# Kernel optimization log

Hardware: AMD Instinct MI355X
Metric: run time of the kernel (lower is better)

Reference implementation:

```python
import jax, jax.numpy as jnp
import numpy as np

B, S, H = 4, 2048, 1024
NH, HD = 16, 64
WIN = 64  # window_size = min(64, seq_len)
SCALE = float(np.sqrt(HD))


def setup_inputs() -> dict:
    key = jax.random.key(0)
    ks = jax.random.split(key, 10)
    w = lambda k, shp: (jax.random.normal(k, shp, jnp.float32) * 0.02)
    return {
        "x": jax.random.normal(ks[0], (B, S, H), jnp.float32),
        "attention_mask": jnp.ones((B, S), jnp.int32),
        "Wq": w(ks[1], (H, NH * HD)), "bq": jnp.zeros((NH * HD,), jnp.float32),
        "Wk": w(ks[2], (H, NH * HD)), "bk": jnp.zeros((NH * HD,), jnp.float32),
        "Wv": w(ks[3], (H, NH * HD)), "bv": jnp.zeros((NH * HD,), jnp.float32),
        "Wo": w(ks[4], (NH * HD, H)), "bo": jnp.zeros((H,), jnp.float32),
    }


def reference(x, attention_mask, Wq, bq, Wk, bk, Wv, bv, Wo, bo):
    # projections -> [B, NH, S, HD]
    def split_heads(t):
        return t.reshape(B, S, NH, HD).transpose(0, 2, 1, 3)
    q = split_heads(x @ Wq + bq)
    k = split_heads(x @ Wk + bk)
    v = split_heads(x @ Wv + bv)

    scores = jnp.einsum("bhqd,bhkd->bhqk", q, k) / SCALE  # [B,NH,S,S]

    # local banded mask: |i - j| <= window_size // 2
    idx = jnp.arange(S)
    local = jnp.abs(idx[None, :] - idx[:, None]) <= (WIN // 2)  # [S,S]
    scores = jnp.where(local[None, None, :, :], scores, -jnp.inf)

    # padding mask: [B,1,1,S]
    scores = jnp.where(attention_mask[:, None, None, :] == 0, -jnp.inf, scores)

    probs = jax.nn.softmax(scores, axis=-1)
    probs = jnp.nan_to_num(probs)  # rows that are fully masked -> 0

    out = jnp.einsum("bhqk,bhkd->bhqd", probs, v)
    out = out.transpose(0, 2, 1, 3).reshape(B, S, NH * HD)
    return out @ Wo + bo
```

## Files before the change

### kernel.cpp

```cpp
#include <hip/hip_runtime.h>
#include <stdint.h>

typedef unsigned short u16;
typedef __attribute__((ext_vector_type(8))) short short8;
typedef __attribute__((ext_vector_type(4))) float f32x4;

#define S_LEN 2048
#define HID   1024
#define QKV_LD 3072
#define M_ROWS 8192

__device__ __forceinline__ u16 f2bf(float f) {
  unsigned u = __float_as_uint(f);
  unsigned r = (u + 0x7fffu + ((u >> 16) & 1u)) >> 16;
  return (u16)r;
}

__device__ __forceinline__ void gload16(const u16* g, u16* l) {
  __builtin_amdgcn_global_load_lds(
      (const __attribute__((address_space(1))) unsigned int*)(g),
      (__attribute__((address_space(3))) unsigned int*)(l),
      16, 0, 0);
}

__global__ __launch_bounds__(256) void cvt_f32_to_bf16(
    const float* __restrict__ in, u16* __restrict__ out, int n) {
  int i = (blockIdx.x * 256 + threadIdx.x) * 8;
  if (i + 8 > n) return;
  float4 a = *(const float4*)(in + i);
  float4 b = *(const float4*)(in + i + 4);
  u16 t[8];
  t[0] = f2bf(a.x); t[1] = f2bf(a.y); t[2] = f2bf(a.z); t[3] = f2bf(a.w);
  t[4] = f2bf(b.x); t[5] = f2bf(b.y); t[6] = f2bf(b.z); t[7] = f2bf(b.w);
  *(short8*)(out + i) = *(short8*)t;
}

__global__ __launch_bounds__(256) void transpose_to_bf16(
    const float* __restrict__ in, u16* __restrict__ out, int K, int N) {
  __shared__ float tile[32][33];
  int tx = threadIdx.x & 31, ty = threadIdx.x >> 5;
  int n0 = blockIdx.x * 32, k0 = blockIdx.y * 32;
#pragma unroll
  for (int i = 0; i < 32; i += 8)
    tile[ty + i][tx] = in[(size_t)(k0 + ty + i) * N + n0 + tx];
  __syncthreads();
#pragma unroll
  for (int i = 0; i < 32; i += 8)
    out[(size_t)(n0 + ty + i) * K + k0 + tx] = f2bf(tile[tx][ty + i]);
}

__global__ __launch_bounds__(256) void pack_bias(
    const float* __restrict__ bq, const float* __restrict__ bk,
    const float* __restrict__ bv, float* __restrict__ out) {
  int i = blockIdx.x * 256 + threadIdx.x;
  if (i >= 3072) return;
  out[i] = (i < 1024) ? bq[i] : (i < 2048) ? bk[i - 1024] : bv[i - 2048];
}

template<int OUT_BF16>
__global__ __launch_bounds__(256, 2) void gemm_bt(
    const u16* __restrict__ A, const u16* __restrict__ Bt,
    const float* __restrict__ bias, void* __restrict__ Cout,
    int M, int N, int K) {
  __shared__ __align__(16) u16 Al[128 * 64];
  __shared__ __align__(16) u16 Bl[128 * 64];
  const int tid = threadIdx.x;
  const int wave = tid >> 6, lane = tid & 63;
  const int nbn = N >> 7;
  int wg = blockIdx.x;
  const int cpx = (int)gridDim.x >> 3;
  wg = (wg & 7) * cpx + (wg >> 3);
  const int bm = wg / nbn, bn = wg % nbn;

  const int wm = wave >> 1, wn = wave & 1;
  const int lrow = lane >> 3;
  const int lslot = lane & 7;
  const int gslot = lslot ^ lrow;
  const int qlane = lane & 15, kgrp = lane >> 4;

  size_t a_off[4], b_off[4];
  u16 *al_base[4], *bl_base[4];
#pragma unroll
  for (int t = 0; t < 4; ++t) {
    int rr = (wave * 4 + t) * 8 + lrow;
    a_off[t] = (size_t)(bm * 128 + rr) * K + gslot * 8;
    b_off[t] = (size_t)(bn * 128 + rr) * K + gslot * 8;
    al_base[t] = Al + (wave * 4 + t) * 512;
    bl_base[t] = Bl + (wave * 4 + t) * 512;
  }

  f32x4 acc[4][4] = {};
  for (int kt = 0; kt < K; kt += 64) {
#pragma unroll
    for (int t = 0; t < 4; ++t) {
      gload16(A + a_off[t] + kt, al_base[t]);
      gload16(Bt + b_off[t] + kt, bl_base[t]);
    }
    __syncthreads();
#pragma unroll
    for (int kk = 0; kk < 2; ++kk) {
      short8 af[4], bf[4];
#pragma unroll
      for (int mf = 0; mf < 4; ++mf) {
        int row = wm * 64 + mf * 16 + qlane;
        int s = (kk * 4 + kgrp) ^ (row & 7);
        af[mf] = *(const short8*)&Al[row * 64 + s * 8];
      }
#pragma unroll
      for (int nf = 0; nf < 4; ++nf) {
        int row = wn * 64 + nf * 16 + qlane;
        int s = (kk * 4 + kgrp) ^ (row & 7);
        bf[nf] = *(const short8*)&Bl[row * 64 + s * 8];
      }
#pragma unroll
      for (int mf = 0; mf < 4; ++mf)
#pragma unroll
        for (int nf = 0; nf < 4; ++nf)
          acc[mf][nf] = __builtin_amdgcn_mfma_f32_16x16x32_bf16(
              af[mf], bf[nf], acc[mf][nf], 0, 0, 0);
    }
    __syncthreads();
  }

#pragma unroll
  for (int nf = 0; nf < 4; ++nf) {
    int col = bn * 128 + wn * 64 + nf * 16 + qlane;
    float bv = bias[col];
#pragma unroll
    for (int mf = 0; mf < 4; ++mf) {
      int row0 = bm * 128 + wm * 64 + mf * 16 + kgrp * 4;
#pragma unroll
      for (int r = 0; r < 4; ++r) {
        float v = acc[mf][nf][r] + bv;
        if (OUT_BF16)
          ((u16*)Cout)[(size_t)(row0 + r) * N + col] = f2bf(v);
        else
          ((float*)Cout)[(size_t)(row0 + r) * N + col] = v;
      }
    }
  }
}

__global__ __launch_bounds__(256, 2) void attn_local(
    const u16* __restrict__ qkv, const int* __restrict__ amask,
    u16* __restrict__ aout) {
  __shared__ __align__(16) u16 Kl[192][72];
  __shared__ __align__(16) u16 Vt[64][200];
  __shared__ __align__(16) u16 Pl[4][32][104];

  const int tid = threadIdx.x, wave = tid >> 6, lane = tid & 63;
  const int qlane = lane & 15, kgrp = lane >> 4;
  const int bz = blockIdx.x;
  const int qt = bz & 15, h = (bz >> 4) & 15, b = bz >> 8;
  const int qs0 = qt * 128;
  const int jt = qs0 - 32;
  const size_t rbase = (size_t)b * S_LEN;

  {
    const int r0 = tid >> 3, c0 = (tid & 7) * 8;
#pragma unroll
    for (int p = 0; p < 6; ++p) {
      int row = p * 32 + r0;
      int j = jt + row;
      u16 kv[8], vv[8];
      if (j >= 0 && j < S_LEN) {
        const u16* kp = qkv + (rbase + j) * QKV_LD + HID + h * 64 + c0;
        *(short8*)kv = *(const short8*)kp;
        *(short8*)vv = *(const short8*)(kp + HID);
      } else {
#pragma unroll
        for (int q = 0; q < 8; ++q) { kv[q] = 0; vv[q] = 0; }
      }
      *(short8*)&Kl[row][c0] = *(short8*)kv;
#pragma unroll
      for (int q = 0; q < 8; ++q) Vt[c0 + q][row] = vv[q];
    }
  }

  short8 qf[2][2];
#pragma unroll
  for (int mf = 0; mf < 2; ++mf)
#pragma unroll
    for (int kk = 0; kk < 2; ++kk)
      qf[mf][kk] = *(const short8*)(qkv +
          (rbase + qs0 + wave * 32 + mf * 16 + qlane) * QKV_LD +
          h * 64 + kk * 32 + kgrp * 8);

  __syncthreads();

  f32x4 sc[2][6] = {};
#pragma unroll
  for (int kk = 0; kk < 2; ++kk) {
    short8 kf[6];
#pragma unroll
    for (int nf = 0; nf < 6; ++nf)
      kf[nf] = *(const short8*)&Kl[wave * 32 + nf * 16 + qlane][kk * 32 + kgrp * 8];
#pragma unroll
    for (int mf = 0; mf < 2; ++mf)
#pragma unroll
      for (int nf = 0; nf < 6; ++nf)
        sc[mf][nf] = __builtin_amdgcn_mfma_f32_16x16x32_bf16(
            qf[mf][kk], kf[nf], sc[mf][nf], 0, 0, 0);
  }

  int jcol[6], mv[6];
#pragma unroll
  for (int nf = 0; nf < 6; ++nf) {
    int j = jt + wave * 32 + nf * 16 + qlane;
    jcol[nf] = j;
    mv[nf] = (j >= 0 && j < S_LEN) ? amask[rbase + j] : 0;
  }

  float inv[2][4];
#pragma unroll
  for (int mf = 0; mf < 2; ++mf) {
    const int irow0 = qs0 + wave * 32 + mf * 16 + kgrp * 4;
    float mx[4] = {-1e30f, -1e30f, -1e30f, -1e30f};
#pragma unroll
    for (int r = 0; r < 4; ++r) {
      int i = irow0 + r;
#pragma unroll
      for (int nf = 0; nf < 6; ++nf) {
        int d = i - jcol[nf];
        if (mv[nf] && d >= -32 && d <= 32) mx[r] = fmaxf(mx[r], sc[mf][nf][r]);
      }
    }
#pragma unroll
    for (int m = 1; m < 16; m <<= 1)
#pragma unroll
      for (int r = 0; r < 4; ++r)
        mx[r] = fmaxf(mx[r], __shfl_xor(mx[r], m));
    float sm[4] = {0.f, 0.f, 0.f, 0.f};
#pragma unroll
    for (int r = 0; r < 4; ++r) {
      int i = irow0 + r;
#pragma unroll
      for (int nf = 0; nf < 6; ++nf) {
        int d = i - jcol[nf];
        bool val = mv[nf] && d >= -32 && d <= 32;
        float p = val ? __expf((sc[mf][nf][r] - mx[r]) * 0.125f) : 0.f;
        sc[mf][nf][r] = p;
        sm[r] += p;
      }
    }
#pragma unroll
    for (int m = 1; m < 16; m <<= 1)
#pragma unroll
      for (int r = 0; r < 4; ++r)
        sm[r] += __shfl_xor(sm[r], m);
#pragma unroll
    for (int r = 0; r < 4; ++r)
      inv[mf][r] = sm[r] > 0.f ? 1.f / sm[r] : 0.f;
#pragma unroll
    for (int nf = 0; nf < 6; ++nf)
#pragma unroll
      for (int r = 0; r < 4; ++r)
        Pl[wave][mf * 16 + kgrp * 4 + r][nf * 16 + qlane] = f2bf(sc[mf][nf][r]);
  }
  __syncthreads();

  f32x4 oc[2][4] = {};
#pragma unroll
  for (int ks = 0; ks < 3; ++ks) {
    short8 pa[2], vb[4];
#pragma unroll
    for (int mf = 0; mf < 2; ++mf)
      pa[mf] = *(const short8*)&Pl[wave][mf * 16 + qlane][ks * 32 + kgrp * 8];
#pragma unroll
    for (int nf = 0; nf < 4; ++nf)
      vb[nf] = *(const short8*)&Vt[nf * 16 + qlane][wave * 32 + ks * 32 + kgrp * 8];
#pragma unroll
    for (int mf = 0; mf < 2; ++mf)
#pragma unroll
      for (int nf = 0; nf < 4; ++nf)
        oc[mf][nf] = __builtin_amdgcn_mfma_f32_16x16x32_bf16(
            pa[mf], vb[nf], oc[mf][nf], 0, 0, 0);
  }

#pragma unroll
  for (int mf = 0; mf < 2; ++mf)
#pragma unroll
    for (int nf = 0; nf < 4; ++nf)
#pragma unroll
      for (int r = 0; r < 4; ++r) {
        size_t row = rbase + qs0 + wave * 32 + mf * 16 + kgrp * 4 + r;
        aout[row * HID + h * 64 + nf * 16 + qlane] =
            f2bf(oc[mf][nf][r] * inv[mf][r]);
      }
}

extern "C" void kernel_launch(void* const* d_in, const int* in_sizes, int n_in,
                              void* d_out, int out_size, void* d_ws, size_t ws_size,
                              hipStream_t stream) {
  const float* x  = (const float*)d_in[0];
  const int* amask = (const int*)d_in[1];
  const float* Wq = (const float*)d_in[2];
  const float* bq = (const float*)d_in[3];
  const float* Wk = (const float*)d_in[4];
  const float* bk = (const float*)d_in[5];
  const float* Wv = (const float*)d_in[6];
  const float* bv = (const float*)d_in[7];
  const float* Wo = (const float*)d_in[8];
  const float* bo = (const float*)d_in[9];
  float* out = (float*)d_out;

  char* w = (char*)d_ws;
  u16* xb    = (u16*)w;   w += (size_t)M_ROWS * HID * 2;
  u16* wqkvt = (u16*)w;   w += (size_t)3072 * 1024 * 2;
  u16* wot   = (u16*)w;   w += (size_t)1024 * 1024 * 2;
  float* bqkv = (float*)w; w += 3072 * 4 + 256;
  u16* qkv   = (u16*)w;   w += (size_t)M_ROWS * 3072 * 2;
  u16* aout  = (u16*)w;   w += (size_t)M_ROWS * HID * 2;

  cvt_f32_to_bf16<<<4096, 256, 0, stream>>>(x, xb, M_ROWS * HID);
  dim3 tg(32, 32);
  transpose_to_bf16<<<tg, 256, 0, stream>>>(Wq, wqkvt,                1024, 1024);
  transpose_to_bf16<<<tg, 256, 0, stream>>>(Wk, wqkvt + 1024 * 1024,  1024, 1024);
  transpose_to_bf16<<<tg, 256, 0, stream>>>(Wv, wqkvt + 2048 * 1024,  1024, 1024);
  transpose_to_bf16<<<tg, 256, 0, stream>>>(Wo, wot,                  1024, 1024);
  pack_bias<<<12, 256, 0, stream>>>(bq, bk, bv, bqkv);

  gemm_bt<1><<<64 * 24, 256, 0, stream>>>(xb, wqkvt, bqkv, qkv, M_ROWS, 3072, 1024);
  attn_local<<<1024, 256, 0, stream>>>(qkv, amask, aout);
  gemm_bt<0><<<64 * 8, 256, 0, stream>>>(aout, wot, bo, out, M_ROWS, 1024, 1024);
}
```

Measured before the change: 131.7 us.

## Rewrite projection GEMMs with 4-stage async LDS pipeline and larger 128x256 tiles

```diff
diff --git a/kernel.cpp b/kernel.cpp
--- a/kernel.cpp
+++ b/kernel.cpp
@@ -21,6 +21,17 @@
       (const __attribute__((address_space(1))) unsigned int*)(g),
       (__attribute__((address_space(3))) unsigned int*)(l),
       16, 0, 0);
+}
+
+template<int N_VM> __device__ __forceinline__ void vmwait() {
+  if constexpr (N_VM == 6)      asm volatile("s_waitcnt vmcnt(6)" ::: "memory");
+  else if constexpr (N_VM == 3) asm volatile("s_waitcnt vmcnt(3)" ::: "memory");
+  else                          asm volatile("s_waitcnt vmcnt(0)" ::: "memory");
+}
+__device__ __forceinline__ void wgbar() {
+  asm volatile("" ::: "memory");
+  __builtin_amdgcn_s_barrier();
+  asm volatile("" ::: "memory");
 }
 
 __global__ __launch_bounds__(256) void cvt_f32_to_bf16(
@@ -58,77 +69,93 @@
 }
 
 template<int OUT_BF16>
-__global__ __launch_bounds__(256, 2) void gemm_bt(
+__global__ __launch_bounds__(512, 2) void gemm_p(
     const u16* __restrict__ A, const u16* __restrict__ Bt,
     const float* __restrict__ bias, void* __restrict__ Cout,
-    int M, int N, int K) {
-  __shared__ __align__(16) u16 Al[128 * 64];
-  __shared__ __align__(16) u16 Bl[128 * 64];
+    int M, int N) {
+  constexpr int K = 1024, NSLAB = 32;
+  constexpr int BM = 128, BN = 256;
+  constexpr int ASL = BM * 32;
+  constexpr int BUFSZ = (BM + BN) * 32;
+  __shared__ __align__(16) u16 smem[4 * BUFSZ];
+
   const int tid = threadIdx.x;
   const int wave = tid >> 6, lane = tid & 63;
-  const int nbn = N >> 7;
+  const int qlane = lane & 15, kgrp = lane >> 4;
+  const int wm = wave >> 2, wn = wave & 3;
+  const int nbn = N >> 8;
   int wg = blockIdx.x;
   const int cpx = (int)gridDim.x >> 3;
   wg = (wg & 7) * cpx + (wg >> 3);
   const int bm = wg / nbn, bn = wg % nbn;
 
-  const int wm = wave >> 1, wn = wave & 1;
-  const int lrow = lane >> 3;
-  const int lslot = lane & 7;
-  const int gslot = lslot ^ lrow;
-  const int qlane = lane & 15, kgrp = lane >> 4;
-
-  size_t a_off[4], b_off[4];
-  u16 *al_base[4], *bl_base[4];
-#pragma unroll
-  for (int t = 0; t < 4; ++t) {
-    int rr = (wave * 4 + t) * 8 + lrow;
-    a_off[t] = (size_t)(bm * 128 + rr) * K + gslot * 8;
-    b_off[t] = (size_t)(bn * 128 + rr) * K + gslot * 8;
-    al_base[t] = Al + (wave * 4 + t) * 512;
-    bl_base[t] = Bl + (wave * 4 + t) * 512;
-  }
+  size_t ga0, gb0, gb1;
+  {
+    int c = tid;
+    int row = c >> 2, sp = c & 3;
+    ga0 = (size_t)(bm * BM + row) * K + (size_t)((sp ^ ((row >> 1) & 3)) * 8);
+  }
+  {
+    int c = tid;
+    int row = c >> 2, sp = c & 3;
+    gb0 = (size_t)(bn * BN + row) * K + (size_t)((sp ^ ((row >> 1) & 3)) * 8);
+    c = tid + 512;
+    row = c >> 2; sp = c & 3;
+    gb1 = (size_t)(bn * BN + row) * K + (size_t)((sp ^ ((row >> 1) & 3)) * 8);
+  }
+
+  auto stage = [&](int t) {
+    const int bb = (t & 3) * BUFSZ;
+    const int kt = t * 32;
+    gload16(A + ga0 + kt,  (u16*)&smem[bb + (wave * 64) * 8]);
+    gload16(Bt + gb0 + kt, (u16*)&smem[bb + ASL + (wave * 64) * 8]);
+    gload16(Bt + gb1 + kt, (u16*)&smem[bb + ASL + (wave * 64 + 512) * 8]);
+  };
 
   f32x4 acc[4][4] = {};
-  for (int kt = 0; kt < K; kt += 64) {
-#pragma unroll
-    for (int t = 0; t < 4; ++t) {
-      gload16(A + a_off[t] + kt, al_base[t]);
-      gload16(Bt + b_off[t] + kt, bl_base[t]);
-    }
-    __syncthreads();
-#pragma unroll
-    for (int kk = 0; kk < 2; ++kk) {
-      short8 af[4], bf[4];
-#pragma unroll
-      for (int mf = 0; mf < 4; ++mf) {
-        int row = wm * 64 + mf * 16 + qlane;
-        int s = (kk * 4 + kgrp) ^ (row & 7);
-        af[mf] = *(const short8*)&Al[row * 64 + s * 8];
-      }
-#pragma unroll
-      for (int nf = 0; nf < 4; ++nf) {
-        int row = wn * 64 + nf * 16 + qlane;
-        int s = (kk * 4 + kgrp) ^ (row & 7);
-        bf[nf] = *(const short8*)&Bl[row * 64 + s * 8];
-      }
-#pragma unroll
-      for (int mf = 0; mf < 4; ++mf)
-#pragma unroll
-        for (int nf = 0; nf < 4; ++nf)
-          acc[mf][nf] = __builtin_amdgcn_mfma_f32_16x16x32_bf16(
-              af[mf], bf[nf], acc[mf][nf], 0, 0, 0);
-    }
-    __syncthreads();
+
+  auto comp = [&](int s) {
+    const u16* Ab = &smem[(s & 3) * BUFSZ];
+    const u16* Bb = Ab + ASL;
+    short8 af[4], bf[4];
+#pragma unroll
+    for (int mf = 0; mf < 4; ++mf) {
+      int r = wm * 64 + mf * 16 + qlane;
+      af[mf] = *(const short8*)&Ab[r * 32 + (kgrp ^ ((r >> 1) & 3)) * 8];
+    }
+#pragma unroll
+    for (int nf = 0; nf < 4; ++nf) {
+      int r = wn * 64 + nf * 16 + qlane;
+      bf[nf] = *(const short8*)&Bb[r * 32 + (kgrp ^ ((r >> 1) & 3)) * 8];
+    }
+    __builtin_amdgcn_s_setprio(1);
+#pragma unroll
+    for (int mf = 0; mf < 4; ++mf)
+#pragma unroll
+      for (int nf = 0; nf < 4; ++nf)
+        acc[mf][nf] = __builtin_amdgcn_mfma_f32_16x16x32_bf16(
+            af[mf], bf[nf], acc[mf][nf], 0, 0, 0);
+    __builtin_amdgcn_s_setprio(0);
+  };
+
+  stage(0); stage(1); stage(2);
+  vmwait<6>();
+  wgbar();
+  for (int s = 0; s < NSLAB; ++s) {
+    if (s + 3 < NSLAB) stage(s + 3);
+    comp(s);
+    if (s + 3 < NSLAB)      { vmwait<6>(); wgbar(); }
+    else if (s + 2 < NSLAB) { vmwait<3>(); wgbar(); }
+    else if (s + 1 < NSLAB) { vmwait<0>(); wgbar(); }
   }
 
 #pragma unroll
   for (int nf = 0; nf < 4; ++nf) {
-    int col = bn * 128 + wn * 64 + nf * 16 + qlane;
+    int col = bn * BN + wn * 64 + nf * 16 + qlane;
     float bv = bias[col];
 #pragma unroll
     for (int mf = 0; mf < 4; ++mf) {
-      int row0 = bm * 128 + wm * 64 + mf * 16 + kgrp * 4;
+      int row0 = bm * BM + wm * 64 + mf * 16 + kgrp * 4;
 #pragma unroll
       for (int r = 0; r < 4; ++r) {
         float v = acc[mf][nf][r] + bv;
@@ -320,7 +347,7 @@
   transpose_to_bf16<<<tg, 256, 0, stream>>>(Wo, wot,                  1024, 1024);
   pack_bias<<<12, 256, 0, stream>>>(bq, bk, bv, bqkv);
 
-  gemm_bt<1><<<64 * 24, 256, 0, stream>>>(xb, wqkvt, bqkv, qkv, M_ROWS, 3072, 1024);
+  gemm_p<1><<<768, 512, 0, stream>>>(xb, wqkvt, bqkv, qkv, M_ROWS, 3072);
   attn_local<<<1024, 256, 0, stream>>>(qkv, amask, aout);
-  gemm_bt<0><<<64 * 8, 256, 0, stream>>>(aout, wot, bo, out, M_ROWS, 1024, 1024);
-}
+  gemm_p<0><<<256, 512, 0, stream>>>(aout, wot, bo, out, M_ROWS, 1024);
+}
```

After: 143.0 us. +8.6%, slower.

## Triple-buffer GEMM with 256x128 tiles, 8 waves, and fuse prep kernels

Applied to the files above, without the earlier changes.

```diff
diff --git a/kernel.cpp b/kernel.cpp
--- a/kernel.cpp
+++ b/kernel.cpp
@@ -23,10 +23,22 @@
       16, 0, 0);
 }
 
-__global__ __launch_bounds__(256) void cvt_f32_to_bf16(
-    const float* __restrict__ in, u16* __restrict__ out, int n) {
+__device__ __forceinline__ void wgbar() {
+  asm volatile("" ::: "memory");
+  __builtin_amdgcn_s_barrier();
+  asm volatile("" ::: "memory");
+}
+
+__global__ __launch_bounds__(256) void cvt_bias(
+    const float* __restrict__ in, u16* __restrict__ out, int n,
+    const float* __restrict__ bq, const float* __restrict__ bk,
+    const float* __restrict__ bv, float* __restrict__ bqkv) {
+  if (blockIdx.x == (unsigned)(n / (256 * 8))) {
+    for (int i = threadIdx.x; i < 3072; i += 256)
+      bqkv[i] = (i < 1024) ? bq[i] : (i < 2048) ? bk[i - 1024] : bv[i - 2048];
+    return;
+  }
   int i = (blockIdx.x * 256 + threadIdx.x) * 8;
-  if (i + 8 > n) return;
   float4 a = *(const float4*)(in + i);
   float4 b = *(const float4*)(in + i + 4);
   u16 t[8];
@@ -35,100 +47,141 @@
   *(short8*)(out + i) = *(short8*)t;
 }
 
-__global__ __launch_bounds__(256) void transpose_to_bf16(
-    const float* __restrict__ in, u16* __restrict__ out, int K, int N) {
+__global__ __launch_bounds__(256) void pack_weights(
+    const float* __restrict__ Wq, const float* __restrict__ Wk,
+    const float* __restrict__ Wv, const float* __restrict__ Wo,
+    u16* __restrict__ wqkvt, u16* __restrict__ wot) {
   __shared__ float tile[32][33];
+  const int z = blockIdx.z;
+  const float* in = (z == 0) ? Wq : (z == 1) ? Wk : (z == 2) ? Wv : Wo;
+  u16* out = (z < 3) ? (wqkvt + (size_t)z * 1024 * 1024) : wot;
   int tx = threadIdx.x & 31, ty = threadIdx.x >> 5;
   int n0 = blockIdx.x * 32, k0 = blockIdx.y * 32;
 #pragma unroll
   for (int i = 0; i < 32; i += 8)
-    tile[ty + i][tx] = in[(size_t)(k0 + ty + i) * N + n0 + tx];
+    tile[ty + i][tx] = in[(size_t)(k0 + ty + i) * 1024 + n0 + tx];
   __syncthreads();
 #pragma unroll
   for (int i = 0; i < 32; i += 8)
-    out[(size_t)(n0 + ty + i) * K + k0 + tx] = f2bf(tile[tx][ty + i]);
-}
-
-__global__ __launch_bounds__(256) void pack_bias(
-    const float* __restrict__ bq, const float* __restrict__ bk,
-    const float* __restrict__ bv, float* __restrict__ out) {
-  int i = blockIdx.x * 256 + threadIdx.x;
-  if (i >= 3072) return;
-  out[i] = (i < 1024) ? bq[i] : (i < 2048) ? bk[i - 1024] : bv[i - 2048];
+    out[(size_t)(n0 + ty + i) * 1024 + k0 + tx] = f2bf(tile[tx][ty + i]);
 }
 
 template<int OUT_BF16>
-__global__ __launch_bounds__(256, 2) void gemm_bt(
+__global__ __launch_bounds__(512, 2) void gemm_p(
     const u16* __restrict__ A, const u16* __restrict__ Bt,
     const float* __restrict__ bias, void* __restrict__ Cout,
-    int M, int N, int K) {
-  __shared__ __align__(16) u16 Al[128 * 64];
-  __shared__ __align__(16) u16 Bl[128 * 64];
+    int M, int N) {
+  constexpr int K = 1024, NT = 16;
+  constexpr int BM = 256, BN = 128;
+  constexpr int AU = BM * 64;
+  constexpr int BUF = (BM + BN) * 64;
+  __shared__ __align__(16) u16 smem[3 * BUF];
+
   const int tid = threadIdx.x;
   const int wave = tid >> 6, lane = tid & 63;
+  const int qlane = lane & 15, kgrp = lane >> 4;
+  const int wm = wave >> 1, wn = wave & 1;
   const int nbn = N >> 7;
   int wg = blockIdx.x;
   const int cpx = (int)gridDim.x >> 3;
   wg = (wg & 7) * cpx + (wg >> 3);
   const int bm = wg / nbn, bn = wg % nbn;
 
-  const int wm = wave >> 1, wn = wave & 1;
-  const int lrow = lane >> 3;
-  const int lslot = lane & 7;
-  const int gslot = lslot ^ lrow;
-  const int qlane = lane & 15, kgrp = lane >> 4;
-
-  size_t a_off[4], b_off[4];
-  u16 *al_base[4], *bl_base[4];
-#pragma unroll
-  for (int t = 0; t < 4; ++t) {
-    int rr = (wave * 4 + t) * 8 + lrow;
-    a_off[t] = (size_t)(bm * 128 + rr) * K + gslot * 8;
-    b_off[t] = (size_t)(bn * 128 + rr) * K + gslot * 8;
-    al_base[t] = Al + (wave * 4 + t) * 512;
-    bl_base[t] = Bl + (wave * 4 + t) * 512;
-  }
+  const int srow = tid >> 3;
+  const int sslot = (tid & 7) ^ (srow & 7);
+  size_t goff[6];
+  int loff[6];
+#pragma unroll
+  for (int u = 0; u < 4; ++u) {
+    goff[u] = (size_t)(bm * BM + u * 64 + srow) * K + sslot * 8;
+    loff[u] = u * 4096 + tid * 8;
+  }
+#pragma unroll
+  for (int u = 0; u < 2; ++u) {
+    goff[4 + u] = (size_t)(bn * BN + u * 64 + srow) * K + sslot * 8;
+    loff[4 + u] = AU + u * 4096 + tid * 8;
+  }
+
+  auto stage = [&](int t, int u) {
+    const u16* g = (u < 4 ? A : Bt) + goff[u] + t * 64;
+    gload16(g, &smem[(t % 3) * BUF + loff[u]]);
+  };
 
   f32x4 acc[4][4] = {};
-  for (int kt = 0; kt < K; kt += 64) {
-#pragma unroll
-    for (int t = 0; t < 4; ++t) {
-      gload16(A + a_off[t] + kt, al_base[t]);
-      gload16(Bt + b_off[t] + kt, bl_base[t]);
-    }
-    __syncthreads();
-#pragma unroll
-    for (int kk = 0; kk < 2; ++kk) {
-      short8 af[4], bf[4];
-#pragma unroll
-      for (int mf = 0; mf < 4; ++mf) {
-        int row = wm * 64 + mf * 16 + qlane;
-        int s = (kk * 4 + kgrp) ^ (row & 7);
-        af[mf] = *(const short8*)&Al[row * 64 + s * 8];
-      }
-#pragma unroll
-      for (int nf = 0; nf < 4; ++nf) {
-        int row = wn * 64 + nf * 16 + qlane;
-        int s = (kk * 4 + kgrp) ^ (row & 7);
-        bf[nf] = *(const short8*)&Bl[row * 64 + s * 8];
-      }
-#pragma unroll
-      for (int mf = 0; mf < 4; ++mf)
-#pragma unroll
-        for (int nf = 0; nf < 4; ++nf)
+
+#pragma unroll
+  for (int u = 0; u < 6; ++u) stage(0, u);
+#pragma unroll
+  for (int u = 0; u < 6; ++u) stage(1, u);
+  asm volatile("s_waitcnt vmcnt(6)" ::: "memory");
+  wgbar();
+
+  for (int t = 0; t < NT; ++t) {
+    const u16* bp = &smem[(t % 3) * BUF];
+    const bool st = (t + 2 < NT);
+    short8 bfr[4][2], afr[2][2];
+
+#pragma unroll
+    for (int mf = 0; mf < 2; ++mf)
+#pragma unroll
+      for (int kk = 0; kk < 2; ++kk) {
+        int r = wm * 64 + mf * 16 + qlane;
+        afr[mf][kk] = *(const short8*)&bp[r * 64 + ((kk * 4 + kgrp) ^ (r & 7)) * 8];
+      }
+#pragma unroll
+    for (int nf = 0; nf < 4; ++nf)
+#pragma unroll
+      for (int kk = 0; kk < 2; ++kk) {
+        int r = wn * 64 + nf * 16 + qlane;
+        bfr[nf][kk] = *(const short8*)&bp[AU + r * 64 + ((kk * 4 + kgrp) ^ (r & 7)) * 8];
+      }
+    if (st) { stage(t + 2, 0); stage(t + 2, 1); stage(t + 2, 2); }
+    wgbar();
+    asm volatile("s_waitcnt lgkmcnt(0)" ::: "memory");
+    __builtin_amdgcn_s_setprio(1);
+#pragma unroll
+    for (int mf = 0; mf < 2; ++mf)
+#pragma unroll
+      for (int nf = 0; nf < 4; ++nf)
+#pragma unroll
+        for (int kk = 0; kk < 2; ++kk)
           acc[mf][nf] = __builtin_amdgcn_mfma_f32_16x16x32_bf16(
-              af[mf], bf[nf], acc[mf][nf], 0, 0, 0);
-    }
-    __syncthreads();
+              afr[mf][kk], bfr[nf][kk], acc[mf][nf], 0, 0, 0);
+    __builtin_amdgcn_s_setprio(0);
+    wgbar();
+
+#pragma unroll
+    for (int mf = 0; mf < 2; ++mf)
+#pragma unroll
+      for (int kk = 0; kk < 2; ++kk) {
+        int r = wm * 64 + (mf + 2) * 16 + qlane;
+        afr[mf][kk] = *(const short8*)&bp[r * 64 + ((kk * 4 + kgrp) ^ (r & 7)) * 8];
+      }
+    if (st) { stage(t + 2, 3); stage(t + 2, 4); stage(t + 2, 5); }
+    wgbar();
+    asm volatile("s_waitcnt lgkmcnt(0)" ::: "memory");
+    __builtin_amdgcn_s_setprio(1);
+#pragma unroll
+    for (int mf = 0; mf < 2; ++mf)
+#pragma unroll
+      for (int nf = 0; nf < 4; ++nf)
+#pragma unroll
+        for (int kk = 0; kk < 2; ++kk)
+          acc[mf + 2][nf] = __builtin_amdgcn_mfma_f32_16x16x32_bf16(
+              afr[mf][kk], bfr[nf][kk], acc[mf + 2][nf], 0, 0, 0);
+    __builtin_amdgcn_s_setprio(0);
+    if (st)                asm volatile("s_waitcnt vmcnt(6)" ::: "memory");
+    else if (t + 1 < NT)   asm volatile("s_waitcnt vmcnt(0)" ::: "memory");
+    if (t + 1 < NT) wgbar();
   }
 
 #pragma unroll
   for (int nf = 0; nf < 4; ++nf) {
-    int col = bn * 128 + wn * 64 + nf * 16 + qlane;
+    int col = bn * BN + wn * 64 + nf * 16 + qlane;
     float bv = bias[col];
 #pragma unroll
     for (int mf = 0; mf < 4; ++mf) {
-      int row0 = bm * 128 + wm * 64 + mf * 16 + kgrp * 4;
+      int row0 = bm * BM + wm * 64 + mf * 16 + kgrp * 4;
 #pragma unroll
       for (int r = 0; r < 4; ++r) {
         float v = acc[mf][nf][r] + bv;
@@ -312,15 +365,10 @@
   u16* qkv   = (u16*)w;   w += (size_t)M_ROWS * 3072 * 2;
   u16* aout  = (u16*)w;   w += (size_t)M_ROWS * HID * 2;
 
-  cvt_f32_to_bf16<<<4096, 256, 0, stream>>>(x, xb, M_ROWS * HID);
-  dim3 tg(32, 32);
-  transpose_to_bf16<<<tg, 256, 0, stream>>>(Wq, wqkvt,                1024, 1024);
-  transpose_to_bf16<<<tg, 256, 0, stream>>>(Wk, wqkvt + 1024 * 1024,  1024, 1024);
-  transpose_to_bf16<<<tg, 256, 0, stream>>>(Wv, wqkvt + 2048 * 1024,  1024, 1024);
-  transpose_to_bf16<<<tg, 256, 0, stream>>>(Wo, wot,                  1024, 1024);
-  pack_bias<<<12, 256, 0, stream>>>(bq, bk, bv, bqkv);
-
-  gemm_bt<1><<<64 * 24, 256, 0, stream>>>(xb, wqkvt, bqkv, qkv, M_ROWS, 3072, 1024);
+  cvt_bias<<<4097, 256, 0, stream>>>(x, xb, M_ROWS * HID, bq, bk, bv, bqkv);
+  pack_weights<<<dim3(32, 32, 4), 256, 0, stream>>>(Wq, Wk, Wv, Wo, wqkvt, wot);
+
+  gemm_p<1><<<768, 512, 0, stream>>>(xb, wqkvt, bqkv, qkv, M_ROWS, 3072);
   attn_local<<<1024, 256, 0, stream>>>(qkv, amask, aout);
-  gemm_bt<0><<<64 * 8, 256, 0, stream>>>(aout, wot, bo, out, M_ROWS, 1024, 1024);
-}
+  gemm_p<0><<<256, 512, 0, stream>>>(aout, wot, bo, out, M_ROWS, 1024);
+}
```

Result: no change. 132.3 us (+0.4%).

## Add dedicated 128x192 pipelined QKV GEMM and merge preprocessing launches

Applied to the files above, without the earlier changes.

```diff
diff --git a/kernel.cpp b/kernel.cpp
--- a/kernel.cpp
+++ b/kernel.cpp
@@ -23,10 +23,22 @@
       16, 0, 0);
 }
 
-__global__ __launch_bounds__(256) void cvt_f32_to_bf16(
-    const float* __restrict__ in, u16* __restrict__ out, int n) {
+__device__ __forceinline__ void wgbar() {
+  asm volatile("" ::: "memory");
+  __builtin_amdgcn_s_barrier();
+  asm volatile("" ::: "memory");
+}
+
+__global__ __launch_bounds__(256) void cvt_bias(
+    const float* __restrict__ in, u16* __restrict__ out, int n,
+    const float* __restrict__ bq, const float* __restrict__ bk,
+    const float* __restrict__ bv, float* __restrict__ bqkv) {
+  if (blockIdx.x == (unsigned)(n / (256 * 8))) {
+    for (int i = threadIdx.x; i < 3072; i += 256)
+      bqkv[i] = (i < 1024) ? bq[i] : (i < 2048) ? bk[i - 1024] : bv[i - 2048];
+    return;
+  }
   int i = (blockIdx.x * 256 + threadIdx.x) * 8;
-  if (i + 8 > n) return;
   float4 a = *(const float4*)(in + i);
   float4 b = *(const float4*)(in + i + 4);
   u16 t[8];
@@ -35,26 +47,169 @@
   *(short8*)(out + i) = *(short8*)t;
 }
 
-__global__ __launch_bounds__(256) void transpose_to_bf16(
-    const float* __restrict__ in, u16* __restrict__ out, int K, int N) {
+__global__ __launch_bounds__(256) void pack_weights(
+    const float* __restrict__ Wq, const float* __restrict__ Wk,
+    const float* __restrict__ Wv, const float* __restrict__ Wo,
+    u16* __restrict__ wqkvt, u16* __restrict__ wot) {
   __shared__ float tile[32][33];
+  const int z = blockIdx.z;
+  const float* in = (z == 0) ? Wq : (z == 1) ? Wk : (z == 2) ? Wv : Wo;
+  u16* out = (z < 3) ? (wqkvt + (size_t)z * 1024 * 1024) : wot;
   int tx = threadIdx.x & 31, ty = threadIdx.x >> 5;
   int n0 = blockIdx.x * 32, k0 = blockIdx.y * 32;
 #pragma unroll
   for (int i = 0; i < 32; i += 8)
-    tile[ty + i][tx] = in[(size_t)(k0 + ty + i) * N + n0 + tx];
+    tile[ty + i][tx] = in[(size_t)(k0 + ty + i) * 1024 + n0 + tx];
   __syncthreads();
 #pragma unroll
   for (int i = 0; i < 32; i += 8)
-    out[(size_t)(n0 + ty + i) * K + k0 + tx] = f2bf(tile[tx][ty + i]);
-}
-
-__global__ __launch_bounds__(256) void pack_bias(
-    const float* __restrict__ bq, const float* __restrict__ bk,
-    const float* __restrict__ bv, float* __restrict__ out) {
-  int i = blockIdx.x * 256 + threadIdx.x;
-  if (i >= 3072) return;
-  out[i] = (i < 1024) ? bq[i] : (i < 2048) ? bk[i - 1024] : bv[i - 2048];
+    out[(size_t)(n0 + ty + i) * 1024 + k0 + tx] = f2bf(tile[tx][ty + i]);
+}
+
+__global__ __launch_bounds__(256, 2) void gemm_k1(
+    const u16* __restrict__ A, const u16* __restrict__ Bt,
+    const float* __restrict__ bias, u16* __restrict__ C, int N) {
+  constexpr int K = 1024, NT = 16;
+  constexpr int BM = 128, BN = 192;
+  constexpr int AU = BM * 64;
+  constexpr int BUF = (BM + BN) * 64;
+  __shared__ __align__(16) u16 smem[2 * BUF];
+
+  const int tid = threadIdx.x;
+  const int wave = tid >> 6, lane = tid & 63;
+  const int qlane = lane & 15, kgrp = lane >> 4;
+  const int wm = wave >> 1, wn = wave & 1;
+  const int nbn = N / BN;
+  int wg = blockIdx.x;
+  const int cpx = (int)gridDim.x >> 3;
+  wg = (wg & 7) * cpx + (wg >> 3);
+  const int bm = wg / nbn, bn = wg % nbn;
+
+  const int srow = tid >> 3;
+  const int sslot = tid & 7;
+  uint32_t gA[4], gB[6];
+#pragma unroll
+  for (int au = 0; au < 4; ++au) {
+    int row = au * 32 + srow;
+    gA[au] = (uint32_t)((bm * BM + row) * K + ((sslot ^ (row & 7)) * 8));
+  }
+#pragma unroll
+  for (int bu = 0; bu < 6; ++bu) {
+    int row = bu * 32 + srow;
+    gB[bu] = (uint32_t)((bn * BN + row) * K + ((sslot ^ (row & 7)) * 8));
+  }
+
+  auto stgA = [&](int t, int au) {
+    gload16(A + (size_t)gA[au] + t * 64, &smem[(t & 1) * BUF + au * 2048 + tid * 8]);
+  };
+  auto stgB = [&](int t, int bu) {
+    gload16(Bt + (size_t)gB[bu] + t * 64, &smem[(t & 1) * BUF + AU + bu * 2048 + tid * 8]);
+  };
+
+#pragma unroll
+  for (int au = 0; au < 4; ++au) stgA(0, au);
+#pragma unroll
+  for (int bu = 0; bu < 6; ++bu) stgB(0, bu);
+#pragma unroll
+  for (int au = 0; au < 4; ++au) stgA(1, au);
+  stgB(1, 0); stgB(1, 1);
+  asm volatile("s_waitcnt vmcnt(6)" ::: "memory");
+  wgbar();
+
+  f32x4 acc[4][6] = {};
+  short8 af[4][2], bf[2][2];
+
+  for (int t = 0; t < NT; ++t) {
+    const u16* bp = &smem[(t & 1) * BUF];
+
+#pragma unroll
+    for (int mf = 0; mf < 4; ++mf)
+#pragma unroll
+      for (int kk = 0; kk < 2; ++kk) {
+        int r = wm * 64 + mf * 16 + qlane;
+        af[mf][kk] = *(const short8*)&bp[r * 64 + ((kk * 4 + kgrp) ^ (r & 7)) * 8];
+      }
+#pragma unroll
+    for (int nf = 0; nf < 2; ++nf)
+#pragma unroll
+      for (int kk = 0; kk < 2; ++kk) {
+        int r = wn * 96 + nf * 16 + qlane;
+        bf[nf][kk] = *(const short8*)&bp[AU + r * 64 + ((kk * 4 + kgrp) ^ (r & 7)) * 8];
+      }
+    if (t + 1 < NT) { stgB(t + 1, 2); stgB(t + 1, 3); stgB(t + 1, 4); stgB(t + 1, 5); }
+    wgbar();
+    asm volatile("s_waitcnt lgkmcnt(0)" ::: "memory");
+    __builtin_amdgcn_s_setprio(1);
+#pragma unroll
+    for (int mf = 0; mf < 4; ++mf)
+#pragma unroll
+      for (int nf = 0; nf < 2; ++nf)
+#pragma unroll
+        for (int kk = 0; kk < 2; ++kk)
+          acc[mf][nf] = __builtin_amdgcn_mfma_f32_16x16x32_bf16(
+              af[mf][kk], bf[nf][kk], acc[mf][nf], 0, 0, 0);
+    __builtin_amdgcn_s_setprio(0);
+    wgbar();
+
+#pragma unroll
+    for (int nf = 0; nf < 2; ++nf)
+#pragma unroll
+      for (int kk = 0; kk < 2; ++kk) {
+        int r = wn * 96 + (nf + 2) * 16 + qlane;
+        bf[nf][kk] = *(const short8*)&bp[AU + r * 64 + ((kk * 4 + kgrp) ^ (r & 7)) * 8];
+      }
+    if (t + 2 < NT) { stgA(t + 2, 0); stgA(t + 2, 1); stgA(t + 2, 2); stgA(t + 2, 3); }
+    wgbar();
+    asm volatile("s_waitcnt lgkmcnt(0)" ::: "memory");
+    __builtin_amdgcn_s_setprio(1);
+#pragma unroll
+    for (int mf = 0; mf < 4; ++mf)
+#pragma unroll
+      for (int nf = 0; nf < 2; ++nf)
+#pragma unroll
+        for (int kk = 0; kk < 2; ++kk)
+          acc[mf][nf + 2] = __builtin_amdgcn_mfma_f32_16x16x32_bf16(
+              af[mf][kk], bf[nf][kk], acc[mf][nf + 2], 0, 0, 0);
+    __builtin_amdgcn_s_setprio(0);
+    wgbar();
+
+#pragma unroll
+    for (int nf = 0; nf < 2; ++nf)
+#pragma unroll
+      for (int kk = 0; kk < 2; ++kk) {
+        int r = wn * 96 + (nf + 4) * 16 + qlane;
+        bf[nf][kk] = *(const short8*)&bp[AU + r * 64 + ((kk * 4 + kgrp) ^ (r & 7)) * 8];
+      }
+    if (t + 2 < NT) { stgB(t + 2, 0); stgB(t + 2, 1); }
+    wgbar();
+    asm volatile("s_waitcnt lgkmcnt(0)" ::: "memory");
+    __builtin_amdgcn_s_setprio(1);
+#pragma unroll
+    for (int mf = 0; mf < 4; ++mf)
+#pragma unroll
+      for (int nf = 0; nf < 2; ++nf)
+#pragma unroll
+        for (int kk = 0; kk < 2; ++kk)
+          acc[mf][nf + 4] = __builtin_amdgcn_mfma_f32_16x16x32_bf16(
+              af[mf][kk], bf[nf][kk], acc[mf][nf + 4], 0, 0, 0);
+    __builtin_amdgcn_s_setprio(0);
+    if (t + 2 < NT)      asm volatile("s_waitcnt vmcnt(6)" ::: "memory");
+    else if (t + 1 < NT) asm volatile("s_waitcnt vmcnt(0)" ::: "memory");
+    if (t + 1 < NT) wgbar();
+  }
+
+#pragma unroll
+  for (int nf = 0; nf < 6; ++nf) {
+    int col = bn * BN + wn * 96 + nf * 16 + qlane;
+    float bv = bias[col];
+#pragma unroll
+    for (int mf = 0; mf < 4; ++mf) {
+      int row0 = bm * BM + wm * 64 + mf * 16 + kgrp * 4;
+#pragma unroll
+      for (int r = 0; r < 4; ++r)
+        C[(size_t)(row0 + r) * N + col] = f2bf(acc[mf][nf][r] + bv);
+    }
+  }
 }
 
 template<int OUT_BF16>
@@ -312,15 +467,10 @@
   u16* qkv   = (u16*)w;   w += (size_t)M_ROWS * 3072 * 2;
   u16* aout  = (u16*)w;   w += (size_t)M_ROWS * HID * 2;
 
-  cvt_f32_to_bf16<<<4096, 256, 0, stream>>>(x, xb, M_ROWS * HID);
-  dim3 tg(32, 32);
-  transpose_to_bf16<<<tg, 256, 0, stream>>>(Wq, wqkvt,                1024, 1024);
-  transpose_to_bf16<<<tg, 256, 0, stream>>>(Wk, wqkvt + 1024 * 1024,  1024, 1024);
-  transpose_to_bf16<<<tg, 256, 0, stream>>>(Wv, wqkvt + 2048 * 1024,  1024, 1024);
-  transpose_to_bf16<<<tg, 256, 0, stream>>>(Wo, wot,                  1024, 1024);
-  pack_bias<<<12, 256, 0, stream>>>(bq, bk, bv, bqkv);
-
-  gemm_bt<1><<<64 * 24, 256, 0, stream>>>(xb, wqkvt, bqkv, qkv, M_ROWS, 3072, 1024);
+  cvt_bias<<<4097, 256, 0, stream>>>(x, xb, M_ROWS * HID, bq, bk, bv, bqkv);
+  pack_weights<<<dim3(32, 32, 4), 256, 0, stream>>>(Wq, Wk, Wv, Wo, wqkvt, wot);
+
+  gemm_k1<<<1024, 256, 0, stream>>>(xb, wqkvt, bqkv, qkv, 3072);
   attn_local<<<1024, 256, 0, stream>>>(qkv, amask, aout);
   gemm_bt<0><<<64 * 8, 256, 0, stream>>>(aout, wot, bo, out, M_ROWS, 1024, 1024);
 }
```

Result: faster. 120.8 us (-8.3%).
